# Optimization experiments

Measured on AMD Instinct MI355X. Metric: run time of the kernel, lower is better.

## Reference

```python
import jax, jax.numpy as jnp
import numpy as np


def setup_inputs() -> dict:
    key = jax.random.key(0)
    k1, k2 = jax.random.split(key)
    B, T, H, F = 8, 768, 128, 10
    context_vectors = jax.random.normal(k1, (B, T, H), dtype=jnp.float32)
    context_matrix = jax.random.normal(k2, (F, H, H), dtype=jnp.float32)
    return {"context_vectors": context_vectors, "context_matrix": context_matrix}


def reference(context_vectors, context_matrix):
    # scores[b,f,i,j] = v_i^T W_f v_j  (bilinear factor scores)
    s = jnp.einsum('bih,fhk,bjk->bfij', context_vectors, context_matrix, context_vectors)
    # original takes argmax over factors then reads that score -> max over f
    scores = jnp.max(s, axis=1)                       # [B, T, T]
    att = jax.nn.softmax(scores, axis=-1)             # softmax over j
    # weighted sum of context vectors
    return jnp.einsum('bij,bjh->bih', att, context_vectors)  # [B, T, H]
```

## Files before the change

kernel.cpp:

```cpp
#include <hip/hip_runtime.h>
#include <hip/hip_bf16.h>

#define B_ 8
#define T_ 768
#define H_ 128
#define F_ 10

using short8v = __attribute__((ext_vector_type(8))) short;
using f32x4   = __attribute__((ext_vector_type(4))) float;

__device__ __forceinline__ float bf2f(unsigned short s) {
  union { unsigned int u; float f; } w;
  w.u = ((unsigned int)s) << 16;
  return w.f;
}
__device__ __forceinline__ unsigned short f2bf(float x) {
  __hip_bfloat16 h = __float2bfloat16(x);
  return *reinterpret_cast<unsigned short*>(&h);
}
union Pk8 { uint4 u4; unsigned short s[8]; };

__global__ __launch_bounds__(256) void r10_PV(const float* __restrict__ V,
                                              unsigned short* __restrict__ VFh,
                                              unsigned short* __restrict__ VFl) {
  const int task = blockIdx.x * 256 + threadIdx.x;
  const int b  = task / (T_ * 16);
  const int r  = task % (T_ * 16);
  const int j  = r >> 4;
  const int ko = r & 15;
  const float* src = V + ((size_t)b * T_ + j) * H_ + ko * 8;
  const float4 v0 = *reinterpret_cast<const float4*>(src);
  const float4 v1 = *reinterpret_cast<const float4*>(src + 4);
  const float vv[8] = {v0.x, v0.y, v0.z, v0.w, v1.x, v1.y, v1.z, v1.w};
  Pk8 hi, lo;
#pragma unroll
  for (int e = 0; e < 8; ++e) {
    const unsigned short h = f2bf(vv[e]);
    hi.s[e] = h;
    lo.s[e] = f2bf(vv[e] - bf2f(h));
  }
  const size_t frag = ((size_t)b * 48 + (j >> 4)) * 4 + (ko >> 2);
  const size_t off = frag * 512 + ((size_t)((j & 15) + 16 * (ko & 3))) * 8;
  *reinterpret_cast<uint4*>(VFh + off) = hi.u4;
  *reinterpret_cast<uint4*>(VFl + off) = lo.u4;
}

__global__ __launch_bounds__(256) void r12_PW2(const float* __restrict__ W,
                                               unsigned short* __restrict__ WFh,
                                               unsigned short* __restrict__ WFl) {
  const int tid = blockIdx.x * 256 + threadIdx.x;
  const int frag = tid >> 6;
  const int l    = tid & 63;
  const int f    = frag >> 5;
  const int rest = frag & 31;
  const int n    = rest >> 2;
  const int ks   = rest & 3;
  const int k  = n * 16 + (l & 15);
  const int h0 = ks * 32 + ((l >> 4) * 8);
  Pk8 hi, lo;
#pragma unroll
  for (int e = 0; e < 8; ++e) {
    const float v = W[((size_t)f * H_ + h0 + e) * H_ + k];
    const unsigned short hh = f2bf(v);
    hi.s[e] = hh;
    lo.s[e] = f2bf(v - bf2f(hh));
  }
  const size_t off = (size_t)frag * 512 + (size_t)l * 8;
  *reinterpret_cast<uint4*>(WFh + off) = hi.u4;
  *reinterpret_cast<uint4*>(WFl + off) = lo.u4;
}

__global__ __launch_bounds__(256) void r12_A(const unsigned short* __restrict__ VFh,
                                             const unsigned short* __restrict__ VFl,
                                             const unsigned short* __restrict__ WFh,
                                             const unsigned short* __restrict__ WFl,
                                             unsigned short* __restrict__ UFh,
                                             unsigned short* __restrict__ UFl) {
  __shared__ __align__(16) float fl[8192];
  const int blk = blockIdx.x;
  const int x     = blk & 7;
  const int local = blk >> 3;
  const int panel = x * 12 + local / 10;
  const int f     = local % 10;
  const int b  = panel / 12;
  const int it = panel % 12;
  const int t  = threadIdx.x;
  const int w  = t >> 6;
  const int l  = t & 63;

  short8v Ah[4], Al[4];
#pragma unroll
  for (int ks = 0; ks < 4; ++ks) {
    const size_t off = (((size_t)b * 48 + it * 4 + w) * 4 + ks) * 512 + (size_t)l * 8;
    Ah[ks] = *reinterpret_cast<const short8v*>(VFh + off);
    Al[ks] = *reinterpret_cast<const short8v*>(VFl + off);
  }

  f32x4 acc[8];
#pragma unroll
  for (int n = 0; n < 8; ++n)
#pragma unroll
    for (int q = 0; q < 4; ++q) acc[n][q] = 0.f;

#pragma unroll
  for (int n = 0; n < 8; ++n)
#pragma unroll
    for (int ks = 0; ks < 4; ++ks) {
      const size_t off = ((size_t)(f * 8 + n) * 4 + ks) * 512 + (size_t)l * 8;
      const short8v bh = *reinterpret_cast<const short8v*>(WFh + off);
      const short8v bl = *reinterpret_cast<const short8v*>(WFl + off);
      acc[n] = __builtin_amdgcn_mfma_f32_16x16x32_bf16(Ah[ks], bh, acc[n], 0, 0, 0);
      acc[n] = __builtin_amdgcn_mfma_f32_16x16x32_bf16(Al[ks], bh, acc[n], 0, 0, 0);
      acc[n] = __builtin_amdgcn_mfma_f32_16x16x32_bf16(Ah[ks], bl, acc[n], 0, 0, 0);
    }

#pragma unroll
  for (int n = 0; n < 8; ++n)
#pragma unroll
    for (int q = 0; q < 4; ++q) {
      const int i_loc = w * 16 + (l >> 4) * 4 + q;
      const int k = n * 16 + (l & 15);
      const int ll = (i_loc & 15) + 16 * ((k >> 3) & 3);
      fl[((w * 4 + (k >> 5)) << 9) + ll * 8 + (k & 7)] = acc[n][q];
    }
  __syncthreads();
  const size_t ufbase = ((size_t)(b * F_ + f) * 192 + it * 16) * 512;
#pragma unroll
  for (int rr = 0; rr < 4; ++rr) {
    const int idx = rr * 2048 + t * 8;
    const float4 v0 = *reinterpret_cast<const float4*>(&fl[idx]);
    const float4 v1 = *reinterpret_cast<const float4*>(&fl[idx + 4]);
    const float vv[8] = {v0.x, v0.y, v0.z, v0.w, v1.x, v1.y, v1.z, v1.w};
    Pk8 hi, lo;
#pragma unroll
    for (int e = 0; e < 8; ++e) {
      const unsigned short h = f2bf(vv[e]);
      hi.s[e] = h;
      lo.s[e] = f2bf(vv[e] - bf2f(h));
    }
    *reinterpret_cast<uint4*>(UFh + ufbase + idx) = hi.u4;
    *reinterpret_cast<uint4*>(UFl + ufbase + idx) = lo.u4;
  }
}

__global__ __launch_bounds__(256) void r10_B(const unsigned short* __restrict__ UFh,
                                             const unsigned short* __restrict__ UFl,
                                             const unsigned short* __restrict__ VFh,
                                             const unsigned short* __restrict__ VFl,
                                             float* __restrict__ S) {
  const int blk = blockIdx.x;
  const int x     = blk & 7;
  const int local = blk >> 3;
  const int panel = x * 12 + local / 12;
  const int jt    = local % 12;
  const int b  = panel / 12;
  const int it = panel % 12;
  const int w  = threadIdx.x >> 6;
  const int l  = threadIdx.x & 63;

  short8v Bh[4][4], Bl[4][4];
#pragma unroll
  for (int n = 0; n < 4; ++n)
#pragma unroll
    for (int ks = 0; ks < 4; ++ks) {
      const size_t off =
          (((size_t)b * 48 + jt * 4 + n) * 4 + ks) * 512 + (size_t)l * 8;
      Bh[n][ks] = *reinterpret_cast<const short8v*>(VFh + off);
      Bl[n][ks] = *reinterpret_cast<const short8v*>(VFl + off);
    }

  f32x4 smax[4];
#pragma unroll
  for (int n = 0; n < 4; ++n)
#pragma unroll
    for (int q = 0; q < 4; ++q) smax[n][q] = -3.4e38f;

  for (int f = 0; f < F_; ++f) {
    const size_t abase = ((size_t)(b * F_ + f) * 48 + it * 4 + w) * 4;
    short8v Ah[4], Al[4];
#pragma unroll
    for (int ks = 0; ks < 4; ++ks) {
      const size_t off = (abase + ks) * 512 + (size_t)l * 8;
      Ah[ks] = *reinterpret_cast<const short8v*>(UFh + off);
      Al[ks] = *reinterpret_cast<const short8v*>(UFl + off);
    }
    f32x4 acc[4];
#pragma unroll
    for (int n = 0; n < 4; ++n)
#pragma unroll
      for (int q = 0; q < 4; ++q) acc[n][q] = 0.f;
#pragma unroll
    for (int ks = 0; ks < 4; ++ks)
#pragma unroll
      for (int n = 0; n < 4; ++n) {
        acc[n] = __builtin_amdgcn_mfma_f32_16x16x32_bf16(Ah[ks], Bh[n][ks], acc[n], 0, 0, 0);
        acc[n] = __builtin_amdgcn_mfma_f32_16x16x32_bf16(Al[ks], Bh[n][ks], acc[n], 0, 0, 0);
        acc[n] = __builtin_amdgcn_mfma_f32_16x16x32_bf16(Ah[ks], Bl[n][ks], acc[n], 0, 0, 0);
      }
#pragma unroll
    for (int n = 0; n < 4; ++n)
#pragma unroll
      for (int q = 0; q < 4; ++q) smax[n][q] = fmaxf(smax[n][q], acc[n][q]);
  }

  const int i0 = it * 64 + w * 16 + (l >> 4) * 4;
  const int j0 = jt * 64 + (l & 15);
#pragma unroll
  for (int n = 0; n < 4; ++n)
#pragma unroll
    for (int q = 0; q < 4; ++q)
      S[((size_t)b * T_ + i0 + q) * T_ + j0 + n * 16] = smax[n][q];
}

__global__ __launch_bounds__(256) void r11_PW(const float* __restrict__ V,
                                              unsigned short* __restrict__ VPh,
                                              unsigned short* __restrict__ VPl) {
  const int tid = blockIdx.x * 256 + threadIdx.x;
  const int h    = tid & 127;
  const int rest = tid >> 7;
  const int jo   = rest % 96;
  const int b    = rest / 96;
  const int j0   = jo * 8;

  Pk8 hi, lo;
#pragma unroll
  for (int e = 0; e < 8; ++e) {
    const float v = V[((size_t)b * T_ + j0 + e) * H_ + h];
    const unsigned short hh = f2bf(v);
    hi.s[e] = hh;
    lo.s[e] = f2bf(v - bf2f(hh));
  }
  const size_t frag = ((size_t)b * 8 + (h >> 4)) * 24 + (j0 >> 5);
  const size_t off = frag * 512 + ((size_t)((h & 15) + 16 * ((j0 >> 3) & 3))) * 8;
  *reinterpret_cast<uint4*>(VPh + off) = hi.u4;
  *reinterpret_cast<uint4*>(VPl + off) = lo.u4;
}

__global__ __launch_bounds__(512) void r15_C(const unsigned short* __restrict__ VPh,
                                             const unsigned short* __restrict__ VPl,
                                             const float* __restrict__ S,
                                             float* __restrict__ O) {
  __shared__ __align__(16) unsigned short sP[16][776];
  __shared__ float sInv[16];
  const int blk = blockIdx.x;
  const int b    = blk & 7;
  const int it16 = blk >> 3;
  const int t  = threadIdx.x;
  const int r  = t >> 5;
  const int c  = t & 31;

  const float* Srow = S + (size_t)(b * T_ + it16 * 16) * T_;

  float4 buf[6];
  float m = -3.4e38f;
#pragma unroll
  for (int q = 0; q < 6; ++q) {
    const int j4 = c + q * 32;
    const float4 x = *reinterpret_cast<const float4*>(&Srow[r * T_ + j4 * 4]);
    buf[q] = x;
    m = fmaxf(m, fmaxf(fmaxf(x.x, x.y), fmaxf(x.z, x.w)));
  }
  m = fmaxf(m, __shfl_xor(m, 1));
  m = fmaxf(m, __shfl_xor(m, 2));
  m = fmaxf(m, __shfl_xor(m, 4));
  m = fmaxf(m, __shfl_xor(m, 8));
  m = fmaxf(m, __shfl_xor(m, 16));

  float l = 0.f;
#pragma unroll
  for (int q = 0; q < 6; ++q) {
    const int j4 = c + q * 32;
    float4 e;
    e.x = expf(buf[q].x - m);
    e.y = expf(buf[q].y - m);
    e.z = expf(buf[q].z - m);
    e.w = expf(buf[q].w - m);
    l += (e.x + e.y) + (e.z + e.w);
    ushort4 pb;
    pb.x = f2bf(e.x); pb.y = f2bf(e.y); pb.z = f2bf(e.z); pb.w = f2bf(e.w);
    *reinterpret_cast<ushort4*>(&sP[r][j4 * 4]) = pb;
  }
  l += __shfl_xor(l, 1);
  l += __shfl_xor(l, 2);
  l += __shfl_xor(l, 4);
  l += __shfl_xor(l, 8);
  l += __shfl_xor(l, 16);
  if (c == 0) sInv[r] = 1.0f / l;
  __syncthreads();

  const int w  = t >> 6;
  const int lv = t & 63;
  f32x4 acc;
#pragma unroll
  for (int q = 0; q < 4; ++q) acc[q] = 0.f;

  const int arow = lv & 15;
  const int koct = lv >> 4;
#pragma unroll
  for (int ks = 0; ks < 24; ++ks) {
    const short8v pa =
        *reinterpret_cast<const short8v*>(&sP[arow][ks * 32 + koct * 8]);
    const size_t f0 = (((size_t)b * 8 + w) * 24 + ks) * 512 + (size_t)lv * 8;
    const short8v vh = *reinterpret_cast<const short8v*>(VPh + f0);
    const short8v vl = *reinterpret_cast<const short8v*>(VPl + f0);
    acc = __builtin_amdgcn_mfma_f32_16x16x32_bf16(pa, vh, acc, 0, 0, 0);
    acc = __builtin_amdgcn_mfma_f32_16x16x32_bf16(pa, vl, acc, 0, 0, 0);
  }

  const int hcol = lv & 15;
#pragma unroll
  for (int q = 0; q < 4; ++q) {
    const int irow = (lv >> 4) * 4 + q;
    const float inv = sInv[irow];
    const size_t obase = ((size_t)(b * T_ + it16 * 16 + irow)) * H_;
    O[obase + w * 16 + hcol] = acc[q] * inv;
  }
}

extern "C" void kernel_launch(void* const* d_in, const int* in_sizes, int n_in,
                              void* d_out, int out_size, void* d_ws, size_t ws_size,
                              hipStream_t stream) {
  const float* V = (const float*)d_in[0];
  const float* W = (const float*)d_in[1];
  if (n_in >= 2 && in_sizes[0] == F_ * H_ * H_) {
    V = (const float*)d_in[1];
    W = (const float*)d_in[0];
  }
  float* O = (float*)d_out;

  const size_t s_bytes  = (size_t)B_ * T_ * T_ * 4;
  const size_t uf_bytes = (size_t)B_ * F_ * H_ * T_ * 2;
  const size_t vf_bytes = (size_t)B_ * H_ * T_ * 2;
  const size_t wf_bytes = (size_t)F_ * H_ * H_ * 2;
  const size_t need = s_bytes + 2 * uf_bytes + 2 * vf_bytes;
  if (ws_size < need) return;

  char* base = (char*)d_ws;
  float* S  = (float*)base;
  unsigned short* WFh = (unsigned short*)base;
  unsigned short* WFl = (unsigned short*)(base + wf_bytes);
  unsigned short* UFh = (unsigned short*)(base + s_bytes);
  unsigned short* UFl = (unsigned short*)(base + s_bytes + uf_bytes);
  unsigned short* VFh = (unsigned short*)(base + s_bytes + 2 * uf_bytes);
  unsigned short* VFl = (unsigned short*)(base + s_bytes + 2 * uf_bytes + vf_bytes);
  unsigned short* VPh = UFh;
  unsigned short* VPl = UFh + vf_bytes / 2;

  r10_PV<<<B_ * T_ * 16 / 256, 256, 0, stream>>>(V, VFh, VFl);
  r12_PW2<<<F_ * 8 * 4 * 64 / 256, 256, 0, stream>>>(W, WFh, WFl);
  r12_A<<<B_ * F_ * (T_ / 64), 256, 0, stream>>>(VFh, VFl, WFh, WFl, UFh, UFl);
  r10_B<<<B_ * (T_ / 64) * (T_ / 64), 256, 0, stream>>>(UFh, UFl, VFh, VFl, S);
  r11_PW<<<B_ * 96 * 128 / 256, 256, 0, stream>>>(V, VPh, VPl);
  r15_C<<<B_ * (T_ / 16), 512, 0, stream>>>(VPh, VPl, S, O);
}
```

Baseline: 79.85 us.

## Split factor loop across two wave groups in score kernel, merge max via LDS

The bilinear score kernel now launches 512 threads per block, and each of two 4-wave groups handles half of the ten factors. The partial maxima are combined through shared memory, and the final tile is written with coalesced float4 stores instead of scattered scalar stores. This doubles the waves per block, which should hide load and MFMA latency and give more parallelism over a serial factor loop. In exchange it adds an LDS round trip and a barrier, and raises register pressure per block, since each wave still holds the full B fragments.

```diff
diff --git a/kernel.cpp b/kernel.cpp
--- a/kernel.cpp
+++ b/kernel.cpp
@@ -143,11 +143,12 @@
   }
 }
 
-__global__ __launch_bounds__(256) void r10_B(const unsigned short* __restrict__ UFh,
+__global__ __launch_bounds__(512) void r16_B(const unsigned short* __restrict__ UFh,
                                              const unsigned short* __restrict__ UFl,
                                              const unsigned short* __restrict__ VFh,
                                              const unsigned short* __restrict__ VFl,
                                              float* __restrict__ S) {
+  __shared__ __align__(16) float sMg[2][4][16][64];
   const int blk = blockIdx.x;
   const int x     = blk & 7;
   const int local = blk >> 3;
@@ -155,8 +156,11 @@
   const int jt    = local % 12;
   const int b  = panel / 12;
   const int it = panel % 12;
-  const int w  = threadIdx.x >> 6;
-  const int l  = threadIdx.x & 63;
+  const int t  = threadIdx.x;
+  const int wid = t >> 6;
+  const int w   = wid & 3;
+  const int g   = wid >> 2;
+  const int l   = t & 63;
 
   short8v Bh[4][4], Bl[4][4];
 #pragma unroll
@@ -175,7 +179,8 @@
 #pragma unroll
     for (int q = 0; q < 4; ++q) smax[n][q] = -3.4e38f;
 
-  for (int f = 0; f < F_; ++f) {
+  for (int fi = 0; fi < 5; ++fi) {
+    const int f = g * 5 + fi;
     const size_t abase = ((size_t)(b * F_ + f) * 48 + it * 4 + w) * 4;
     short8v Ah[4], Al[4];
 #pragma unroll
@@ -203,13 +208,28 @@
       for (int q = 0; q < 4; ++q) smax[n][q] = fmaxf(smax[n][q], acc[n][q]);
   }
 
-  const int i0 = it * 64 + w * 16 + (l >> 4) * 4;
-  const int j0 = jt * 64 + (l & 15);
 #pragma unroll
   for (int n = 0; n < 4; ++n)
 #pragma unroll
     for (int q = 0; q < 4; ++q)
-      S[((size_t)b * T_ + i0 + q) * T_ + j0 + n * 16] = smax[n][q];
+      sMg[g][w][(l >> 4) * 4 + q][(l & 15) + 16 * n] = smax[n][q];
+  __syncthreads();
+
+  const int w2  = t >> 7;
+  const int rem = t & 127;
+  const int row = rem >> 3;
+  const int c8  = (rem & 7) * 8;
+  const float4 a0 = *reinterpret_cast<const float4*>(&sMg[0][w2][row][c8]);
+  const float4 a1 = *reinterpret_cast<const float4*>(&sMg[0][w2][row][c8 + 4]);
+  const float4 b0 = *reinterpret_cast<const float4*>(&sMg[1][w2][row][c8]);
+  const float4 b1 = *reinterpret_cast<const float4*>(&sMg[1][w2][row][c8 + 4]);
+  float4 o0 = make_float4(fmaxf(a0.x, b0.x), fmaxf(a0.y, b0.y),
+                          fmaxf(a0.z, b0.z), fmaxf(a0.w, b0.w));
+  float4 o1 = make_float4(fmaxf(a1.x, b1.x), fmaxf(a1.y, b1.y),
+                          fmaxf(a1.z, b1.z), fmaxf(a1.w, b1.w));
+  float* dst = S + ((size_t)b * T_ + it * 64 + w2 * 16 + row) * T_ + jt * 64 + c8;
+  *reinterpret_cast<float4*>(dst)     = o0;
+  *reinterpret_cast<float4*>(dst + 4) = o1;
 }
 
 __global__ __launch_bounds__(256) void r11_PW(const float* __restrict__ V,
@@ -349,7 +369,7 @@
   r10_PV<<<B_ * T_ * 16 / 256, 256, 0, stream>>>(V, VFh, VFl);
   r12_PW2<<<F_ * 8 * 4 * 64 / 256, 256, 0, stream>>>(W, WFh, WFl);
   r12_A<<<B_ * F_ * (T_ / 64), 256, 0, stream>>>(VFh, VFl, WFh, WFl, UFh, UFl);
-  r10_B<<<B_ * (T_ / 64) * (T_ / 64), 256, 0, stream>>>(UFh, UFl, VFh, VFl, S);
+  r16_B<<<B_ * (T_ / 64) * (T_ / 64), 512, 0, stream>>>(UFh, UFl, VFh, VFl, S);
   r11_PW<<<B_ * 96 * 128 / 256, 256, 0, stream>>>(V, VPh, VPl);
   r15_C<<<B_ * (T_ / 16), 512, 0, stream>>>(VPh, VPl, S, O);
 }
```

Measured after the change: 90.72 us. 1.14x slower.

## Split score kernel columns across two wave groups and prefetch next factor's A tiles

Applied to the files above, without the earlier changes.

The score kernel now launches 512 threads per block. Two groups of four waves each compute half of the 64 output columns, which halves the per-thread B fragments and accumulators. The A fragments for factor f+1 are double-buffered in registers and loaded while factor f runs its MFMAs, so global load latency overlaps with compute. The split raises wave count and lowers register pressure per wave, but every A tile is now fetched by both wave groups, doubling A traffic from L2.

```diff
diff --git a/kernel.cpp b/kernel.cpp
--- a/kernel.cpp
+++ b/kernel.cpp
@@ -143,7 +143,7 @@
   }
 }
 
-__global__ __launch_bounds__(256) void r10_B(const unsigned short* __restrict__ UFh,
+__global__ __launch_bounds__(512) void r17_B(const unsigned short* __restrict__ UFh,
                                              const unsigned short* __restrict__ UFl,
                                              const unsigned short* __restrict__ VFh,
                                              const unsigned short* __restrict__ VFl,
@@ -155,61 +155,78 @@
   const int jt    = local % 12;
   const int b  = panel / 12;
   const int it = panel % 12;
-  const int w  = threadIdx.x >> 6;
-  const int l  = threadIdx.x & 63;
-
-  short8v Bh[4][4], Bl[4][4];
-#pragma unroll
-  for (int n = 0; n < 4; ++n)
+  const int t  = threadIdx.x;
+  const int wid = t >> 6;
+  const int w   = wid & 3;
+  const int g   = wid >> 2;
+  const int l   = t & 63;
+
+  short8v Bh[2][4], Bl[2][4];
+#pragma unroll
+  for (int n2 = 0; n2 < 2; ++n2)
 #pragma unroll
     for (int ks = 0; ks < 4; ++ks) {
       const size_t off =
-          (((size_t)b * 48 + jt * 4 + n) * 4 + ks) * 512 + (size_t)l * 8;
-      Bh[n][ks] = *reinterpret_cast<const short8v*>(VFh + off);
-      Bl[n][ks] = *reinterpret_cast<const short8v*>(VFl + off);
-    }
-
-  f32x4 smax[4];
-#pragma unroll
-  for (int n = 0; n < 4; ++n)
-#pragma unroll
-    for (int q = 0; q < 4; ++q) smax[n][q] = -3.4e38f;
-
+          (((size_t)b * 48 + jt * 4 + (g * 2 + n2)) * 4 + ks) * 512 + (size_t)l * 8;
+      Bh[n2][ks] = *reinterpret_cast<const short8v*>(VFh + off);
+      Bl[n2][ks] = *reinterpret_cast<const short8v*>(VFl + off);
+    }
+
+  f32x4 smax[2];
+#pragma unroll
+  for (int n2 = 0; n2 < 2; ++n2)
+#pragma unroll
+    for (int q = 0; q < 4; ++q) smax[n2][q] = -3.4e38f;
+
+  short8v Ah[2][4], Al[2][4];
+#pragma unroll
+  for (int ks = 0; ks < 4; ++ks) {
+    const size_t off =
+        (((size_t)(b * F_ + 0) * 48 + it * 4 + w) * 4 + ks) * 512 + (size_t)l * 8;
+    Ah[0][ks] = *reinterpret_cast<const short8v*>(UFh + off);
+    Al[0][ks] = *reinterpret_cast<const short8v*>(UFl + off);
+  }
+
+#pragma unroll
   for (int f = 0; f < F_; ++f) {
-    const size_t abase = ((size_t)(b * F_ + f) * 48 + it * 4 + w) * 4;
-    short8v Ah[4], Al[4];
-#pragma unroll
-    for (int ks = 0; ks < 4; ++ks) {
-      const size_t off = (abase + ks) * 512 + (size_t)l * 8;
-      Ah[ks] = *reinterpret_cast<const short8v*>(UFh + off);
-      Al[ks] = *reinterpret_cast<const short8v*>(UFl + off);
-    }
-    f32x4 acc[4];
-#pragma unroll
-    for (int n = 0; n < 4; ++n)
-#pragma unroll
-      for (int q = 0; q < 4; ++q) acc[n][q] = 0.f;
+    const int cur = f & 1;
+    const int nxt = cur ^ 1;
+    if (f + 1 < F_) {
+#pragma unroll
+      for (int ks = 0; ks < 4; ++ks) {
+        const size_t off =
+            (((size_t)(b * F_ + f + 1) * 48 + it * 4 + w) * 4 + ks) * 512 +
+            (size_t)l * 8;
+        Ah[nxt][ks] = *reinterpret_cast<const short8v*>(UFh + off);
+        Al[nxt][ks] = *reinterpret_cast<const short8v*>(UFl + off);
+      }
+    }
+    f32x4 acc[2];
+#pragma unroll
+    for (int n2 = 0; n2 < 2; ++n2)
+#pragma unroll
+      for (int q = 0; q < 4; ++q) acc[n2][q] = 0.f;
 #pragma unroll
     for (int ks = 0; ks < 4; ++ks)
 #pragma unroll
-      for (int n = 0; n < 4; ++n) {
-        acc[n] = __builtin_amdgcn_mfma_f32_16x16x32_bf16(Ah[ks], Bh[n][ks], acc[n], 0, 0, 0);
-        acc[n] = __builtin_amdgcn_mfma_f32_16x16x32_bf16(Al[ks], Bh[n][ks], acc[n], 0, 0, 0);
-        acc[n] = __builtin_amdgcn_mfma_f32_16x16x32_bf16(Ah[ks], Bl[n][ks], acc[n], 0, 0, 0);
+      for (int n2 = 0; n2 < 2; ++n2) {
+        acc[n2] = __builtin_amdgcn_mfma_f32_16x16x32_bf16(Ah[cur][ks], Bh[n2][ks], acc[n2], 0, 0, 0);
+        acc[n2] = __builtin_amdgcn_mfma_f32_16x16x32_bf16(Al[cur][ks], Bh[n2][ks], acc[n2], 0, 0, 0);
+        acc[n2] = __builtin_amdgcn_mfma_f32_16x16x32_bf16(Ah[cur][ks], Bl[n2][ks], acc[n2], 0, 0, 0);
       }
 #pragma unroll
-    for (int n = 0; n < 4; ++n)
-#pragma unroll
-      for (int q = 0; q < 4; ++q) smax[n][q] = fmaxf(smax[n][q], acc[n][q]);
+    for (int n2 = 0; n2 < 2; ++n2)
+#pragma unroll
+      for (int q = 0; q < 4; ++q) smax[n2][q] = fmaxf(smax[n2][q], acc[n2][q]);
   }
 
   const int i0 = it * 64 + w * 16 + (l >> 4) * 4;
-  const int j0 = jt * 64 + (l & 15);
-#pragma unroll
-  for (int n = 0; n < 4; ++n)
+  const int j0 = jt * 64 + g * 32 + (l & 15);
+#pragma unroll
+  for (int n2 = 0; n2 < 2; ++n2)
 #pragma unroll
     for (int q = 0; q < 4; ++q)
-      S[((size_t)b * T_ + i0 + q) * T_ + j0 + n * 16] = smax[n][q];
+      S[((size_t)b * T_ + i0 + q) * T_ + j0 + n2 * 16] = smax[n2][q];
 }
 
 __global__ __launch_bounds__(256) void r11_PW(const float* __restrict__ V,
@@ -349,7 +366,7 @@
   r10_PV<<<B_ * T_ * 16 / 256, 256, 0, stream>>>(V, VFh, VFl);
   r12_PW2<<<F_ * 8 * 4 * 64 / 256, 256, 0, stream>>>(W, WFh, WFl);
   r12_A<<<B_ * F_ * (T_ / 64), 256, 0, stream>>>(VFh, VFl, WFh, WFl, UFh, UFl);
-  r10_B<<<B_ * (T_ / 64) * (T_ / 64), 256, 0, stream>>>(UFh, UFl, VFh, VFl, S);
+  r17_B<<<B_ * (T_ / 64) * (T_ / 64), 512, 0, stream>>>(UFh, UFl, VFh, VFl, S);
   r11_PW<<<B_ * 96 * 128 / 256, 256, 0, stream>>>(V, VPh, VPl);
   r15_C<<<B_ * (T_ / 16), 512, 0, stream>>>(VPh, VPl, S, O);
 }
```

Measured after the change: 84.55 us. 1.06x slower.

## Merge three prep kernels into one launch, add setprio and dual accumulators

Applied to the files above, without the earlier changes.

The V fragment, W fragment and transposed-V packing kernels are combined into one kernel that branches on block index. To make this possible, workspace buffers for VP and WF get their own regions instead of aliasing S/UF, so the transposed-V packing can run before the score kernels. This removes two kernel launches and their gaps. The change also wraps the MFMA loops in s_setprio and splits the PV accumulation across two independent accumulators to shorten the MFMA dependency chain. The cost is a larger workspace requirement.

```diff
diff --git a/kernel.cpp b/kernel.cpp
--- a/kernel.cpp
+++ b/kernel.cpp
@@ -20,54 +20,77 @@
 }
 union Pk8 { uint4 u4; unsigned short s[8]; };
 
-__global__ __launch_bounds__(256) void r10_PV(const float* __restrict__ V,
-                                              unsigned short* __restrict__ VFh,
-                                              unsigned short* __restrict__ VFl) {
-  const int task = blockIdx.x * 256 + threadIdx.x;
-  const int b  = task / (T_ * 16);
-  const int r  = task % (T_ * 16);
-  const int j  = r >> 4;
-  const int ko = r & 15;
-  const float* src = V + ((size_t)b * T_ + j) * H_ + ko * 8;
-  const float4 v0 = *reinterpret_cast<const float4*>(src);
-  const float4 v1 = *reinterpret_cast<const float4*>(src + 4);
-  const float vv[8] = {v0.x, v0.y, v0.z, v0.w, v1.x, v1.y, v1.z, v1.w};
-  Pk8 hi, lo;
-#pragma unroll
-  for (int e = 0; e < 8; ++e) {
-    const unsigned short h = f2bf(vv[e]);
-    hi.s[e] = h;
-    lo.s[e] = f2bf(vv[e] - bf2f(h));
-  }
-  const size_t frag = ((size_t)b * 48 + (j >> 4)) * 4 + (ko >> 2);
-  const size_t off = frag * 512 + ((size_t)((j & 15) + 16 * (ko & 3))) * 8;
-  *reinterpret_cast<uint4*>(VFh + off) = hi.u4;
-  *reinterpret_cast<uint4*>(VFl + off) = lo.u4;
-}
-
-__global__ __launch_bounds__(256) void r12_PW2(const float* __restrict__ W,
-                                               unsigned short* __restrict__ WFh,
-                                               unsigned short* __restrict__ WFl) {
-  const int tid = blockIdx.x * 256 + threadIdx.x;
-  const int frag = tid >> 6;
-  const int l    = tid & 63;
-  const int f    = frag >> 5;
-  const int rest = frag & 31;
-  const int n    = rest >> 2;
-  const int ks   = rest & 3;
-  const int k  = n * 16 + (l & 15);
-  const int h0 = ks * 32 + ((l >> 4) * 8);
-  Pk8 hi, lo;
-#pragma unroll
-  for (int e = 0; e < 8; ++e) {
-    const float v = W[((size_t)f * H_ + h0 + e) * H_ + k];
-    const unsigned short hh = f2bf(v);
-    hi.s[e] = hh;
-    lo.s[e] = f2bf(v - bf2f(hh));
-  }
-  const size_t off = (size_t)frag * 512 + (size_t)l * 8;
-  *reinterpret_cast<uint4*>(WFh + off) = hi.u4;
-  *reinterpret_cast<uint4*>(WFl + off) = lo.u4;
+__global__ __launch_bounds__(256) void r18_P(const float* __restrict__ V,
+                                             const float* __restrict__ W,
+                                             unsigned short* __restrict__ VFh,
+                                             unsigned short* __restrict__ VFl,
+                                             unsigned short* __restrict__ WFh,
+                                             unsigned short* __restrict__ WFl,
+                                             unsigned short* __restrict__ VPh,
+                                             unsigned short* __restrict__ VPl) {
+  const int blk = blockIdx.x;
+  if (blk < 384) {
+    const int task = blk * 256 + threadIdx.x;
+    const int b  = task / (T_ * 16);
+    const int r  = task % (T_ * 16);
+    const int j  = r >> 4;
+    const int ko = r & 15;
+    const float* src = V + ((size_t)b * T_ + j) * H_ + ko * 8;
+    const float4 v0 = *reinterpret_cast<const float4*>(src);
+    const float4 v1 = *reinterpret_cast<const float4*>(src + 4);
+    const float vv[8] = {v0.x, v0.y, v0.z, v0.w, v1.x, v1.y, v1.z, v1.w};
+    Pk8 hi, lo;
+#pragma unroll
+    for (int e = 0; e < 8; ++e) {
+      const unsigned short h = f2bf(vv[e]);
+      hi.s[e] = h;
+      lo.s[e] = f2bf(vv[e] - bf2f(h));
+    }
+    const size_t frag = ((size_t)b * 48 + (j >> 4)) * 4 + (ko >> 2);
+    const size_t off = frag * 512 + ((size_t)((j & 15) + 16 * (ko & 3))) * 8;
+    *reinterpret_cast<uint4*>(VFh + off) = hi.u4;
+    *reinterpret_cast<uint4*>(VFl + off) = lo.u4;
+  } else if (blk < 464) {
+    const int tid = (blk - 384) * 256 + threadIdx.x;
+    const int frag = tid >> 6;
+    const int l    = tid & 63;
+    const int f    = frag >> 5;
+    const int rest = frag & 31;
+    const int n    = rest >> 2;
+    const int ks   = rest & 3;
+    const int k  = n * 16 + (l & 15);
+    const int h0 = ks * 32 + ((l >> 4) * 8);
+    Pk8 hi, lo;
+#pragma unroll
+    for (int e = 0; e < 8; ++e) {
+      const float v = W[((size_t)f * H_ + h0 + e) * H_ + k];
+      const unsigned short hh = f2bf(v);
+      hi.s[e] = hh;
+      lo.s[e] = f2bf(v - bf2f(hh));
+    }
+    const size_t off = (size_t)frag * 512 + (size_t)l * 8;
+    *reinterpret_cast<uint4*>(WFh + off) = hi.u4;
+    *reinterpret_cast<uint4*>(WFl + off) = lo.u4;
+  } else {
+    const int tid = (blk - 464) * 256 + threadIdx.x;
+    const int h    = tid & 127;
+    const int rest = tid >> 7;
+    const int jo   = rest % 96;
+    const int b    = rest / 96;
+    const int j0   = jo * 8;
+    Pk8 hi, lo;
+#pragma unroll
+    for (int e = 0; e < 8; ++e) {
+      const float v = V[((size_t)b * T_ + j0 + e) * H_ + h];
+      const unsigned short hh = f2bf(v);
+      hi.s[e] = hh;
+      lo.s[e] = f2bf(v - bf2f(hh));
+    }
+    const size_t frag = ((size_t)b * 8 + (h >> 4)) * 24 + (j0 >> 5);
+    const size_t off = frag * 512 + ((size_t)((h & 15) + 16 * ((j0 >> 3) & 3))) * 8;
+    *reinterpret_cast<uint4*>(VPh + off) = hi.u4;
+    *reinterpret_cast<uint4*>(VPl + off) = lo.u4;
+  }
 }
 
 __global__ __launch_bounds__(256) void r12_A(const unsigned short* __restrict__ VFh,
@@ -189,6 +212,7 @@
     for (int n = 0; n < 4; ++n)
 #pragma unroll
       for (int q = 0; q < 4; ++q) acc[n][q] = 0.f;
+    __builtin_amdgcn_s_setprio(1);
 #pragma unroll
     for (int ks = 0; ks < 4; ++ks)
 #pragma unroll
@@ -197,6 +221,7 @@
         acc[n] = __builtin_amdgcn_mfma_f32_16x16x32_bf16(Al[ks], Bh[n][ks], acc[n], 0, 0, 0);
         acc[n] = __builtin_amdgcn_mfma_f32_16x16x32_bf16(Ah[ks], Bl[n][ks], acc[n], 0, 0, 0);
       }
+    __builtin_amdgcn_s_setprio(0);
 #pragma unroll
     for (int n = 0; n < 4; ++n)
 #pragma unroll
@@ -212,31 +237,7 @@
       S[((size_t)b * T_ + i0 + q) * T_ + j0 + n * 16] = smax[n][q];
 }
 
-__global__ __launch_bounds__(256) void r11_PW(const float* __restrict__ V,
-                                              unsigned short* __restrict__ VPh,
-                                              unsigned short* __restrict__ VPl) {
-  const int tid = blockIdx.x * 256 + threadIdx.x;
-  const int h    = tid & 127;
-  const int rest = tid >> 7;
-  const int jo   = rest % 96;
-  const int b    = rest / 96;
-  const int j0   = jo * 8;
-
-  Pk8 hi, lo;
-#pragma unroll
-  for (int e = 0; e < 8; ++e) {
-    const float v = V[((size_t)b * T_ + j0 + e) * H_ + h];
-    const unsigned short hh = f2bf(v);
-    hi.s[e] = hh;
-    lo.s[e] = f2bf(v - bf2f(hh));
-  }
-  const size_t frag = ((size_t)b * 8 + (h >> 4)) * 24 + (j0 >> 5);
-  const size_t off = frag * 512 + ((size_t)((h & 15) + 16 * ((j0 >> 3) & 3))) * 8;
-  *reinterpret_cast<uint4*>(VPh + off) = hi.u4;
-  *reinterpret_cast<uint4*>(VPl + off) = lo.u4;
-}
-
-__global__ __launch_bounds__(512) void r15_C(const unsigned short* __restrict__ VPh,
+__global__ __launch_bounds__(512) void r18_C(const unsigned short* __restrict__ VPh,
                                              const unsigned short* __restrict__ VPl,
                                              const float* __restrict__ S,
                                              float* __restrict__ O) {
@@ -290,22 +291,33 @@
 
   const int w  = t >> 6;
   const int lv = t & 63;
-  f32x4 acc;
-#pragma unroll
-  for (int q = 0; q < 4; ++q) acc[q] = 0.f;
+  f32x4 acc0, acc1;
+#pragma unroll
+  for (int q = 0; q < 4; ++q) { acc0[q] = 0.f; acc1[q] = 0.f; }
 
   const int arow = lv & 15;
   const int koct = lv >> 4;
-#pragma unroll
-  for (int ks = 0; ks < 24; ++ks) {
-    const short8v pa =
-        *reinterpret_cast<const short8v*>(&sP[arow][ks * 32 + koct * 8]);
-    const size_t f0 = (((size_t)b * 8 + w) * 24 + ks) * 512 + (size_t)lv * 8;
-    const short8v vh = *reinterpret_cast<const short8v*>(VPh + f0);
-    const short8v vl = *reinterpret_cast<const short8v*>(VPl + f0);
-    acc = __builtin_amdgcn_mfma_f32_16x16x32_bf16(pa, vh, acc, 0, 0, 0);
-    acc = __builtin_amdgcn_mfma_f32_16x16x32_bf16(pa, vl, acc, 0, 0, 0);
-  }
+  __builtin_amdgcn_s_setprio(1);
+#pragma unroll
+  for (int ks2 = 0; ks2 < 12; ++ks2) {
+    const int ksA = ks2 * 2;
+    const int ksB = ks2 * 2 + 1;
+    const short8v paA =
+        *reinterpret_cast<const short8v*>(&sP[arow][ksA * 32 + koct * 8]);
+    const short8v paB =
+        *reinterpret_cast<const short8v*>(&sP[arow][ksB * 32 + koct * 8]);
+    const size_t fA = (((size_t)b * 8 + w) * 24 + ksA) * 512 + (size_t)lv * 8;
+    const size_t fB = (((size_t)b * 8 + w) * 24 + ksB) * 512 + (size_t)lv * 8;
+    const short8v vhA = *reinterpret_cast<const short8v*>(VPh + fA);
+    const short8v vlA = *reinterpret_cast<const short8v*>(VPl + fA);
+    const short8v vhB = *reinterpret_cast<const short8v*>(VPh + fB);
+    const short8v vlB = *reinterpret_cast<const short8v*>(VPl + fB);
+    acc0 = __builtin_amdgcn_mfma_f32_16x16x32_bf16(paA, vhA, acc0, 0, 0, 0);
+    acc1 = __builtin_amdgcn_mfma_f32_16x16x32_bf16(paB, vhB, acc1, 0, 0, 0);
+    acc0 = __builtin_amdgcn_mfma_f32_16x16x32_bf16(paA, vlA, acc0, 0, 0, 0);
+    acc1 = __builtin_amdgcn_mfma_f32_16x16x32_bf16(paB, vlB, acc1, 0, 0, 0);
+  }
+  __builtin_amdgcn_s_setprio(0);
 
   const int hcol = lv & 15;
 #pragma unroll
@@ -313,7 +325,7 @@
     const int irow = (lv >> 4) * 4 + q;
     const float inv = sInv[irow];
     const size_t obase = ((size_t)(b * T_ + it16 * 16 + irow)) * H_;
-    O[obase + w * 16 + hcol] = acc[q] * inv;
+    O[obase + w * 16 + hcol] = (acc0[q] + acc1[q]) * inv;
   }
 }
 
@@ -332,24 +344,22 @@
   const size_t uf_bytes = (size_t)B_ * F_ * H_ * T_ * 2;
   const size_t vf_bytes = (size_t)B_ * H_ * T_ * 2;
   const size_t wf_bytes = (size_t)F_ * H_ * H_ * 2;
-  const size_t need = s_bytes + 2 * uf_bytes + 2 * vf_bytes;
+  const size_t need = s_bytes + 2 * uf_bytes + 4 * vf_bytes + 2 * wf_bytes;
   if (ws_size < need) return;
 
   char* base = (char*)d_ws;
   float* S  = (float*)base;
-  unsigned short* WFh = (unsigned short*)base;
-  unsigned short* WFl = (unsigned short*)(base + wf_bytes);
   unsigned short* UFh = (unsigned short*)(base + s_bytes);
   unsigned short* UFl = (unsigned short*)(base + s_bytes + uf_bytes);
   unsigned short* VFh = (unsigned short*)(base + s_bytes + 2 * uf_bytes);
   unsigned short* VFl = (unsigned short*)(base + s_bytes + 2 * uf_bytes + vf_bytes);
-  unsigned short* VPh = UFh;
-  unsigned short* VPl = UFh + vf_bytes / 2;
-
-  r10_PV<<<B_ * T_ * 16 / 256, 256, 0, stream>>>(V, VFh, VFl);
-  r12_PW2<<<F_ * 8 * 4 * 64 / 256, 256, 0, stream>>>(W, WFh, WFl);
+  unsigned short* VPh = (unsigned short*)(base + s_bytes + 2 * uf_bytes + 2 * vf_bytes);
+  unsigned short* VPl = (unsigned short*)(base + s_bytes + 2 * uf_bytes + 3 * vf_bytes);
+  unsigned short* WFh = (unsigned short*)(base + s_bytes + 2 * uf_bytes + 4 * vf_bytes);
+  unsigned short* WFl = (unsigned short*)(base + s_bytes + 2 * uf_bytes + 4 * vf_bytes + wf_bytes);
+
+  r18_P<<<848, 256, 0, stream>>>(V, W, VFh, VFl, WFh, WFl, VPh, VPl);
   r12_A<<<B_ * F_ * (T_ / 64), 256, 0, stream>>>(VFh, VFl, WFh, WFl, UFh, UFl);
   r10_B<<<B_ * (T_ / 64) * (T_ / 64), 256, 0, stream>>>(UFh, UFl, VFh, VFl, S);
-  r11_PW<<<B_ * 96 * 128 / 256, 256, 0, stream>>>(V, VPh, VPl);
-  r15_C<<<B_ * (T_ / 16), 512, 0, stream>>>(VPh, VPl, S, O);
-}
+  r18_C<<<B_ * (T_ / 16), 512, 0, stream>>>(VPh, VPl, S, O);
+}
```

After: 71.74 us. 1.11x faster.
